# Performance work log

Measured on AMD Instinct MI355X. Metric: run time of the kernel, lower is better.

Reference implementation:

```python
import jax, jax.numpy as jnp
import numpy as np

N_NODES = 50000
N_EDGES = 800000
IN_DIM = 128
HID_DIM = 128
OUT_DIM = 128


def gcn_conv(x, src, dst, W, b, n):
    """PyG-style GCNConv: linear, add self-loops, sym-normalized scatter-add."""
    h = x @ W  # [N, out]
    loop = jnp.arange(n, dtype=src.dtype)
    src_f = jnp.concatenate([src, loop])
    dst_f = jnp.concatenate([dst, loop])
    ones = jnp.ones(src_f.shape[0], dtype=h.dtype)
    deg = jax.ops.segment_sum(ones, dst_f, num_segments=n)  # in-degree incl. self-loop
    dinv = jnp.where(deg > 0, jax.lax.rsqrt(deg), 0.0)
    norm = dinv[src_f] * dinv[dst_f]  # [E+N]
    msg = h[src_f] * norm[:, None]  # gather + scale
    out = jax.ops.segment_sum(msg, dst_f, num_segments=n)  # scatter-add
    return out + b


def setup_inputs() -> dict:
    key = jax.random.key(0)
    k1, k2, k3, k4, k5, k6 = jax.random.split(key, 6)
    posts = jax.random.normal(k1, (N_NODES, IN_DIM), dtype=jnp.float32)
    edge_index = jax.random.randint(k2, (2, N_EDGES), 0, N_NODES, dtype=jnp.int32)
    root_index = 0
    s1 = 1.0 / np.sqrt(IN_DIM)
    s2 = 1.0 / np.sqrt(HID_DIM + IN_DIM)
    W1 = jax.random.uniform(k3, (IN_DIM, HID_DIM), jnp.float32, -s1, s1)
    b1 = jax.random.uniform(k4, (HID_DIM,), jnp.float32, -s1, s1)
    W2 = jax.random.uniform(k5, (HID_DIM + IN_DIM, OUT_DIM), jnp.float32, -s2, s2)
    b2 = jax.random.uniform(k6, (OUT_DIM,), jnp.float32, -s2, s2)
    return {"posts": posts, "edge_index": edge_index, "root_index": root_index,
            "W1": W1, "b1": b1, "W2": W2, "b2": b2}


def reference(posts, edge_index, root_index, W1, b1, W2, b2):
    n = posts.shape[0]
    src, dst = edge_index[0], edge_index[1]
    post_root = posts[root_index]  # [in_dim], broadcast to all nodes below
    conv1_out = gcn_conv(posts, src, dst, W1, b1, n)  # [N, hid]
    conv1_root = conv1_out[root_index]  # [hid]
    conv2_in = jnp.concatenate(
        [jnp.broadcast_to(post_root, (n, post_root.shape[0])), conv1_out], axis=1)
    conv2_in = jax.nn.relu(conv2_in)  # dropout is identity in eval mode
    conv2_out = jax.nn.relu(gcn_conv(conv2_in, src, dst, W2, b2, n))  # [N, out]
    # mean over nodes of cat([conv1_root broadcast, conv2_out])
    feature = jnp.concatenate([conv1_root, jnp.mean(conv2_out, axis=0)])
    return feature.reshape(1, -1)
```

## Files before the change

kernel.cpp:

```cpp
#include <hip/hip_runtime.h>

#define DIM 128
#define WPAD 136
typedef unsigned int uint;
typedef unsigned short ushort;

#define RFL __builtin_amdgcn_readfirstlane

typedef __attribute__((ext_vector_type(8))) short bf16x8;
typedef __attribute__((ext_vector_type(4))) float f32x4;

__device__ __forceinline__ ushort f2bf(float x) {
    uint u = __float_as_uint(x);
    u = u + 0x7FFFu + ((u >> 16) & 1u);
    return (ushort)(u >> 16);
}

__global__ __launch_bounds__(256) void k_count(const int* __restrict__ dst,
                                               int* __restrict__ deg, int E) {
    int t = blockIdx.x * 256 + threadIdx.x;
    if (t < E) atomicAdd(&deg[dst[t]], 1);
}

__global__ __launch_bounds__(256) void k_dinv(const int* __restrict__ deg,
                                              float* __restrict__ dinv, int N) {
    int t = blockIdx.x * 256 + threadIdx.x;
    if (t < N) dinv[t] = rsqrtf((float)(deg[t] + 1));
}

__global__ __launch_bounds__(256) void k_scanA(const int* __restrict__ deg,
                                               int* __restrict__ rowptr,
                                               int* __restrict__ segsum, int N) {
    int i = blockIdx.x * 256 + threadIdx.x;
    int v = (i < N) ? deg[i] : 0;
    __shared__ int ps[256];
    ps[threadIdx.x] = v;
    __syncthreads();
    for (int off = 1; off < 256; off <<= 1) {
        int u = (threadIdx.x >= off) ? ps[threadIdx.x - off] : 0;
        __syncthreads();
        ps[threadIdx.x] += u;
        __syncthreads();
    }
    if (i < N) rowptr[i] = ps[threadIdx.x] - v;
    if (threadIdx.x == 255) segsum[blockIdx.x] = ps[255];
}

__global__ __launch_bounds__(256) void k_scanB(int* __restrict__ segsum, int nseg) {
    int t = threadIdx.x;
    int v = (t < nseg) ? segsum[t] : 0;
    __shared__ int ps[256];
    ps[t] = v;
    __syncthreads();
    for (int off = 1; off < 256; off <<= 1) {
        int u = (t >= off) ? ps[t - off] : 0;
        __syncthreads();
        ps[t] += u;
        __syncthreads();
    }
    if (t < nseg) segsum[t] = ps[t] - v;
}

__global__ __launch_bounds__(256) void k_scanC(int* __restrict__ rowptr,
                                               const int* __restrict__ segsum,
                                               int* __restrict__ cursor, int N, int E) {
    int i = blockIdx.x * 256 + threadIdx.x;
    if (i < N) {
        int r = rowptr[i] + segsum[blockIdx.x];
        rowptr[i] = r;
        cursor[i] = r;
    }
    if (i == 0) rowptr[N] = E;
}

__global__ __launch_bounds__(256) void k_fill(const int* __restrict__ src,
                                              const int* __restrict__ dst,
                                              const float* __restrict__ dinv,
                                              int* __restrict__ cursor,
                                              int2* __restrict__ csr, int E) {
    int e = blockIdx.x * 256 + threadIdx.x;
    if (e >= E) return;
    int s = src[e], d = dst[e];
    int p = atomicAdd(&cursor[d], 1);
    float w = dinv[s] * dinv[d];
    csr[p] = make_int2(s, __float_as_int(w));
}

template<bool RELU_IN, bool ADD_C>
__global__ __launch_bounds__(256) void k_gemm(const float* __restrict__ X,
                                              const float* __restrict__ W,
                                              const float* __restrict__ Cvec,
                                              ushort* __restrict__ H, int n) {
    __shared__ ushort sWT[DIM][WPAD];
    __shared__ ushort sX[4][16][WPAD];
    const int tid = threadIdx.x;
    const int w = tid >> 6, l = tid & 63;
    const int col = l & 15;
    const int kg = l >> 4;

    for (int idx = tid; idx < DIM * DIM; idx += 256) {
        int k = idx >> 7, j = idx & 127;
        sWT[j][k] = f2bf(W[idx]);
    }
    float cj[8];
    if (ADD_C) {
        #pragma unroll
        for (int t = 0; t < 8; ++t) cj[t] = Cvec[t * 16 + col];
    }
    __syncthreads();

    for (int base = blockIdx.x * 64; base < n; base += gridDim.x * 64) {
        int i0 = base + w * 16;
        for (int idx = l; idx < 16 * 32; idx += 64) {
            int r = idx >> 5, c4 = idx & 31;
            float4 v = make_float4(0.f, 0.f, 0.f, 0.f);
            if (i0 + r < n) v = ((const float4*)(X + (size_t)(i0 + r) * DIM))[c4];
            if (RELU_IN) {
                v.x = fmaxf(v.x, 0.f); v.y = fmaxf(v.y, 0.f);
                v.z = fmaxf(v.z, 0.f); v.w = fmaxf(v.w, 0.f);
            }
            ushort* p = &sX[w][r][c4 * 4];
            p[0] = f2bf(v.x); p[1] = f2bf(v.y); p[2] = f2bf(v.z); p[3] = f2bf(v.w);
        }
        f32x4 acc[8];
        #pragma unroll
        for (int t = 0; t < 8; ++t) {
            float c0 = ADD_C ? cj[t] : 0.f;
            acc[t][0] = c0; acc[t][1] = c0; acc[t][2] = c0; acc[t][3] = c0;
        }
        #pragma unroll
        for (int k0 = 0; k0 < DIM; k0 += 32) {
            bf16x8 a = *(const bf16x8*)&sX[w][col][k0 + kg * 8];
            #pragma unroll
            for (int t = 0; t < 8; ++t) {
                bf16x8 b = *(const bf16x8*)&sWT[t * 16 + col][k0 + kg * 8];
                acc[t] = __builtin_amdgcn_mfma_f32_16x16x32_bf16(a, b, acc[t], 0, 0, 0);
            }
        }
        #pragma unroll
        for (int t = 0; t < 8; ++t) {
            #pragma unroll
            for (int r = 0; r < 4; ++r) {
                int row = i0 + kg * 4 + r;
                if (row < n) H[(size_t)row * DIM + t * 16 + col] = f2bf(acc[t][r]);
            }
        }
    }
}

__global__ __launch_bounds__(DIM) void k_cvec(const float* __restrict__ posts,
                                              const int* __restrict__ root,
                                              const float* __restrict__ W2,
                                              float* __restrict__ cvec) {
    int j = threadIdx.x;
    const float* xr = posts + (size_t)root[0] * DIM;
    float acc = 0.0f;
    #pragma unroll 8
    for (int k = 0; k < DIM; ++k)
        acc = fmaf(fmaxf(xr[k], 0.0f), W2[k * DIM + j], acc);
    cvec[j] = acc;
}

__device__ __forceinline__ void wave_accum(const int2* __restrict__ csr,
                                           int beg, int end, int q,
                                           const ushort* __restrict__ h,
                                           float& a0, float& a1) {
    int e = beg;
    for (; e + 16 <= end; e += 16) {
        int sc[16];
        float wt[16];
        #pragma unroll
        for (int u = 0; u < 16; ++u) {
            int2 c = csr[e + u];
            sc[u] = RFL(c.x);
            wt[u] = __int_as_float(RFL(c.y));
        }
        uint hv[16];
        #pragma unroll
        for (int u = 0; u < 16; ++u)
            hv[u] = ((const uint*)(h + (size_t)sc[u] * DIM))[q];
        #pragma unroll
        for (int u = 0; u < 16; ++u) {
            a0 = fmaf(__uint_as_float(hv[u] << 16), wt[u], a0);
            a1 = fmaf(__uint_as_float(hv[u] & 0xFFFF0000u), wt[u], a1);
        }
    }
    for (; e + 8 <= end; e += 8) {
        int sc[8];
        float wt[8];
        #pragma unroll
        for (int u = 0; u < 8; ++u) {
            int2 c = csr[e + u];
            sc[u] = RFL(c.x);
            wt[u] = __int_as_float(RFL(c.y));
        }
        uint hv[8];
        #pragma unroll
        for (int u = 0; u < 8; ++u)
            hv[u] = ((const uint*)(h + (size_t)sc[u] * DIM))[q];
        #pragma unroll
        for (int u = 0; u < 8; ++u) {
            a0 = fmaf(__uint_as_float(hv[u] << 16), wt[u], a0);
            a1 = fmaf(__uint_as_float(hv[u] & 0xFFFF0000u), wt[u], a1);
        }
    }
    int rem = end - e;
    if (rem > 0) {
        int sc[8];
        float wt[8];
        #pragma unroll
        for (int u = 0; u < 8; ++u) {
            int idx = e + u; idx = idx < end ? idx : end - 1;
            int2 c = csr[idx];
            sc[u] = RFL(c.x);
            wt[u] = (u < rem) ? __int_as_float(RFL(c.y)) : 0.f;
        }
        uint hv[8];
        #pragma unroll
        for (int u = 0; u < 8; ++u)
            hv[u] = ((const uint*)(h + (size_t)sc[u] * DIM))[q];
        #pragma unroll
        for (int u = 0; u < 8; ++u) {
            a0 = fmaf(__uint_as_float(hv[u] << 16), wt[u], a0);
            a1 = fmaf(__uint_as_float(hv[u] & 0xFFFF0000u), wt[u], a1);
        }
    }
}

__global__ __launch_bounds__(256) void k_gather1(const int2* __restrict__ csr,
                                                 const int* __restrict__ rowptr,
                                                 const float* __restrict__ dinv,
                                                 const ushort* __restrict__ h,
                                                 const float* __restrict__ b1,
                                                 const int* __restrict__ root,
                                                 float* __restrict__ conv1,
                                                 float* __restrict__ out, int N) {
    int q = threadIdx.x & 63;
    int wid = blockIdx.x * 4 + (threadIdx.x >> 6);
    int wstride = gridDim.x * 4;
    float2 bv = ((const float2*)b1)[q];
    int rt = RFL(root[0]);
    for (int d = wid; d < N; d += wstride) {
        int beg = RFL(rowptr[d]);
        int end = RFL(rowptr[d + 1]);
        float a0 = 0.f, a1 = 0.f;
        wave_accum(csr, beg, end, q, h, a0, a1);
        float di = dinv[d], sl = di * di;
        uint hv = ((const uint*)(h + (size_t)d * DIM))[q];
        float2 r;
        r.x = fmaf(__uint_as_float(hv << 16), sl, a0) + bv.x;
        r.y = fmaf(__uint_as_float(hv & 0xFFFF0000u), sl, a1) + bv.y;
        ((float2*)(conv1 + (size_t)d * DIM))[q] = r;
        if (d == rt) ((float2*)out)[q] = r;
    }
}

__global__ __launch_bounds__(256) void k_gather2(const int2* __restrict__ csr,
                                                 const int* __restrict__ rowptr,
                                                 const float* __restrict__ dinv,
                                                 const ushort* __restrict__ h,
                                                 const float* __restrict__ b2,
                                                 float* __restrict__ meanacc, int N) {
    int q = threadIdx.x & 63;
    int wid = blockIdx.x * 4 + (threadIdx.x >> 6);
    int wstride = gridDim.x * 4;
    float2 bv = ((const float2*)b2)[q];
    float s0 = 0.f, s1 = 0.f;
    for (int d = wid; d < N; d += wstride) {
        int beg = RFL(rowptr[d]);
        int end = RFL(rowptr[d + 1]);
        float a0 = 0.f, a1 = 0.f;
        wave_accum(csr, beg, end, q, h, a0, a1);
        float di = dinv[d], sl = di * di;
        uint hv = ((const uint*)(h + (size_t)d * DIM))[q];
        s0 += fmaxf(fmaf(__uint_as_float(hv << 16), sl, a0) + bv.x, 0.f);
        s1 += fmaxf(fmaf(__uint_as_float(hv & 0xFFFF0000u), sl, a1) + bv.y, 0.f);
    }
    __shared__ float2 sp[256];
    sp[threadIdx.x] = make_float2(s0, s1);
    __syncthreads();
    if (threadIdx.x < 64) {
        float2 s = sp[threadIdx.x];
        #pragma unroll
        for (int g = 1; g < 4; ++g) {
            float2 o = sp[g * 64 + threadIdx.x];
            s.x += o.x; s.y += o.y;
        }
        unsafeAtomicAdd(&meanacc[q * 2 + 0], s.x);
        unsafeAtomicAdd(&meanacc[q * 2 + 1], s.y);
    }
}

__global__ __launch_bounds__(DIM) void k_reduce(const float* __restrict__ meanacc,
                                                float* __restrict__ out, int N) {
    int j = threadIdx.x;
    out[DIM + j] = meanacc[j] / (float)N;
}

extern "C" void kernel_launch(void* const* d_in, const int* in_sizes, int n_in,
                              void* d_out, int out_size, void* d_ws, size_t ws_size,
                              hipStream_t stream) {
    const float* posts = (const float*)d_in[0];
    const int*   eidx  = (const int*)d_in[1];
    const int*   root  = (const int*)d_in[2];
    const float* W1    = (const float*)d_in[3];
    const float* b1    = (const float*)d_in[4];
    const float* W2    = (const float*)d_in[5];
    const float* b2    = (const float*)d_in[6];
    float* out = (float*)d_out;

    int N = in_sizes[0] / DIM;
    int E = in_sizes[1] / 2;
    const int* src = eidx;
    const int* dst = eidx + E;
    int nseg = (N + 255) / 256;

    char* ws = (char*)d_ws;
    size_t off = 0;
    auto alloc = [&](size_t bytes) {
        void* p = ws + off;
        off += (bytes + 511) & ~(size_t)511;
        return p;
    };
    int*    deg     = (int*)   alloc((size_t)N * 4);
    int*    rowptr  = (int*)   alloc((size_t)(N + 1) * 4);
    int*    cursor  = (int*)   alloc((size_t)N * 4);
    int*    segsum  = (int*)   alloc((size_t)nseg * 4);
    float*  dinv    = (float*) alloc((size_t)N * 4);
    float*  cvec    = (float*) alloc(DIM * 4);
    float*  meanacc = (float*) alloc(DIM * 4);
    int2*   csr     = (int2*)  alloc((size_t)E * 8);
    ushort* h       = (ushort*)alloc((size_t)N * DIM * 2);
    float*  conv1   = (float*) alloc((size_t)N * DIM * 4);

    hipMemsetAsync(deg, 0, (size_t)N * 4, stream);
    hipMemsetAsync(meanacc, 0, DIM * 4, stream);

    k_count<<<(E + 255) / 256, 256, 0, stream>>>(dst, deg, E);
    k_scanA<<<nseg, 256, 0, stream>>>(deg, rowptr, segsum, N);
    k_scanB<<<1, 256, 0, stream>>>(segsum, nseg);
    k_scanC<<<nseg, 256, 0, stream>>>(rowptr, segsum, cursor, N, E);
    k_dinv<<<(N + 255) / 256, 256, 0, stream>>>(deg, dinv, N);
    k_fill<<<(E + 255) / 256, 256, 0, stream>>>(src, dst, dinv, cursor, csr, E);

    k_gemm<false, false><<<256, 256, 0, stream>>>(posts, W1, nullptr, h, N);
    k_gather1<<<2048, 256, 0, stream>>>(csr, rowptr, dinv, h, b1, root, conv1, out, N);

    k_cvec<<<1, DIM, 0, stream>>>(posts, root, W2, cvec);
    k_gemm<true, true><<<256, 256, 0, stream>>>(conv1, W2 + DIM * DIM, cvec, h, N);
    k_gather2<<<2048, 256, 0, stream>>>(csr, rowptr, dinv, h, b2, meanacc, N);
    k_reduce<<<1, DIM, 0, stream>>>(meanacc, out, N);
}
```

Before: 302.9 us.

## Partition CSR edges by source quarter and gather in four cache-friendly passes

Edges are bucketed per destination by which quarter of the node range their source falls in. Each gather then runs as four passes, each touching only one quarter of the bf16 feature table, which is meant to keep gather reads resident in cache. The cost is four times the launches, a partial accumulator row read and written in fp32 between passes, and a four-times-larger degree/scan array. k_scanB now needs 1024 threads to cover the larger segment count.

```diff
diff --git a/kernel.cpp b/kernel.cpp
--- a/kernel.cpp
+++ b/kernel.cpp
@@ -16,23 +16,35 @@
     return (ushort)(u >> 16);
 }
 
-__global__ __launch_bounds__(256) void k_count(const int* __restrict__ dst,
-                                               int* __restrict__ deg, int E) {
+__device__ __forceinline__ int src_bucket(int s, int Q) {
+    int p = s / Q;
+    return p > 3 ? 3 : p;
+}
+
+__global__ __launch_bounds__(256) void k_count4(const int* __restrict__ src,
+                                                const int* __restrict__ dst,
+                                                int* __restrict__ deg4, int E, int Q) {
     int t = blockIdx.x * 256 + threadIdx.x;
-    if (t < E) atomicAdd(&deg[dst[t]], 1);
-}
-
-__global__ __launch_bounds__(256) void k_dinv(const int* __restrict__ deg,
+    if (t < E) {
+        int p = src_bucket(src[t], Q);
+        atomicAdd(&deg4[(dst[t] << 2) + p], 1);
+    }
+}
+
+__global__ __launch_bounds__(256) void k_dinv(const int* __restrict__ rowptr4,
                                               float* __restrict__ dinv, int N) {
     int t = blockIdx.x * 256 + threadIdx.x;
-    if (t < N) dinv[t] = rsqrtf((float)(deg[t] + 1));
+    if (t < N) {
+        int deg = rowptr4[(t << 2) + 4] - rowptr4[t << 2];
+        dinv[t] = rsqrtf((float)(deg + 1));
+    }
 }
 
 __global__ __launch_bounds__(256) void k_scanA(const int* __restrict__ deg,
                                                int* __restrict__ rowptr,
-                                               int* __restrict__ segsum, int N) {
+                                               int* __restrict__ segsum, int M) {
     int i = blockIdx.x * 256 + threadIdx.x;
-    int v = (i < N) ? deg[i] : 0;
+    int v = (i < M) ? deg[i] : 0;
     __shared__ int ps[256];
     ps[threadIdx.x] = v;
     __syncthreads();
@@ -42,17 +54,17 @@
         ps[threadIdx.x] += u;
         __syncthreads();
     }
-    if (i < N) rowptr[i] = ps[threadIdx.x] - v;
+    if (i < M) rowptr[i] = ps[threadIdx.x] - v;
     if (threadIdx.x == 255) segsum[blockIdx.x] = ps[255];
 }
 
-__global__ __launch_bounds__(256) void k_scanB(int* __restrict__ segsum, int nseg) {
+__global__ __launch_bounds__(1024) void k_scanB(int* __restrict__ segsum, int nseg) {
     int t = threadIdx.x;
     int v = (t < nseg) ? segsum[t] : 0;
-    __shared__ int ps[256];
+    __shared__ int ps[1024];
     ps[t] = v;
     __syncthreads();
-    for (int off = 1; off < 256; off <<= 1) {
+    for (int off = 1; off < 1024; off <<= 1) {
         int u = (t >= off) ? ps[t - off] : 0;
         __syncthreads();
         ps[t] += u;
@@ -63,27 +75,28 @@
 
 __global__ __launch_bounds__(256) void k_scanC(int* __restrict__ rowptr,
                                                const int* __restrict__ segsum,
-                                               int* __restrict__ cursor, int N, int E) {
+                                               int* __restrict__ cursor, int M, int E) {
     int i = blockIdx.x * 256 + threadIdx.x;
-    if (i < N) {
+    if (i < M) {
         int r = rowptr[i] + segsum[blockIdx.x];
         rowptr[i] = r;
         cursor[i] = r;
     }
-    if (i == 0) rowptr[N] = E;
-}
-
-__global__ __launch_bounds__(256) void k_fill(const int* __restrict__ src,
-                                              const int* __restrict__ dst,
-                                              const float* __restrict__ dinv,
-                                              int* __restrict__ cursor,
-                                              int2* __restrict__ csr, int E) {
+    if (i == 0) rowptr[M] = E;
+}
+
+__global__ __launch_bounds__(256) void k_fill4(const int* __restrict__ src,
+                                               const int* __restrict__ dst,
+                                               const float* __restrict__ dinv,
+                                               int* __restrict__ cursor4,
+                                               int2* __restrict__ csr, int E, int Q) {
     int e = blockIdx.x * 256 + threadIdx.x;
     if (e >= E) return;
     int s = src[e], d = dst[e];
-    int p = atomicAdd(&cursor[d], 1);
+    int p = src_bucket(s, Q);
+    int pos = atomicAdd(&cursor4[(d << 2) + p], 1);
     float w = dinv[s] * dinv[d];
-    csr[p] = make_int2(s, __float_as_int(w));
+    csr[pos] = make_int2(s, __float_as_int(w));
 }
 
 template<bool RELU_IN, bool ADD_C>
@@ -227,67 +240,91 @@
     }
 }
 
+template<bool FIRST, bool LAST>
 __global__ __launch_bounds__(256) void k_gather1(const int2* __restrict__ csr,
-                                                 const int* __restrict__ rowptr,
+                                                 const int* __restrict__ rowptr4,
                                                  const float* __restrict__ dinv,
                                                  const ushort* __restrict__ h,
                                                  const float* __restrict__ b1,
                                                  const int* __restrict__ root,
                                                  float* __restrict__ conv1,
-                                                 float* __restrict__ out, int N) {
+                                                 float* __restrict__ out, int N, int pass) {
     int q = threadIdx.x & 63;
     int wid = blockIdx.x * 4 + (threadIdx.x >> 6);
     int wstride = gridDim.x * 4;
     float2 bv = ((const float2*)b1)[q];
     int rt = RFL(root[0]);
     for (int d = wid; d < N; d += wstride) {
-        int beg = RFL(rowptr[d]);
-        int end = RFL(rowptr[d + 1]);
+        int idx = (d << 2) + pass;
+        int beg = RFL(rowptr4[idx]);
+        int end = RFL(rowptr4[idx + 1]);
         float a0 = 0.f, a1 = 0.f;
         wave_accum(csr, beg, end, q, h, a0, a1);
-        float di = dinv[d], sl = di * di;
-        uint hv = ((const uint*)(h + (size_t)d * DIM))[q];
-        float2 r;
-        r.x = fmaf(__uint_as_float(hv << 16), sl, a0) + bv.x;
-        r.y = fmaf(__uint_as_float(hv & 0xFFFF0000u), sl, a1) + bv.y;
-        ((float2*)(conv1 + (size_t)d * DIM))[q] = r;
-        if (d == rt) ((float2*)out)[q] = r;
-    }
-}
-
+        float2* crow = (float2*)(conv1 + (size_t)d * DIM) + q;
+        float2 r = make_float2(a0, a1);
+        if (!FIRST) {
+            float2 c = *crow;
+            r.x += c.x; r.y += c.y;
+        }
+        if (LAST) {
+            float di = dinv[d], sl = di * di;
+            uint hv = ((const uint*)(h + (size_t)d * DIM))[q];
+            r.x = fmaf(__uint_as_float(hv << 16), sl, r.x) + bv.x;
+            r.y = fmaf(__uint_as_float(hv & 0xFFFF0000u), sl, r.y) + bv.y;
+        }
+        *crow = r;
+        if (LAST && d == rt) ((float2*)out)[q] = r;
+    }
+}
+
+template<bool FIRST, bool LAST>
 __global__ __launch_bounds__(256) void k_gather2(const int2* __restrict__ csr,
-                                                 const int* __restrict__ rowptr,
+                                                 const int* __restrict__ rowptr4,
                                                  const float* __restrict__ dinv,
                                                  const ushort* __restrict__ h,
                                                  const float* __restrict__ b2,
-                                                 float* __restrict__ meanacc, int N) {
+                                                 float* __restrict__ acc2,
+                                                 float* __restrict__ meanacc, int N, int pass) {
     int q = threadIdx.x & 63;
     int wid = blockIdx.x * 4 + (threadIdx.x >> 6);
     int wstride = gridDim.x * 4;
     float2 bv = ((const float2*)b2)[q];
     float s0 = 0.f, s1 = 0.f;
     for (int d = wid; d < N; d += wstride) {
-        int beg = RFL(rowptr[d]);
-        int end = RFL(rowptr[d + 1]);
+        int idx = (d << 2) + pass;
+        int beg = RFL(rowptr4[idx]);
+        int end = RFL(rowptr4[idx + 1]);
         float a0 = 0.f, a1 = 0.f;
         wave_accum(csr, beg, end, q, h, a0, a1);
-        float di = dinv[d], sl = di * di;
-        uint hv = ((const uint*)(h + (size_t)d * DIM))[q];
-        s0 += fmaxf(fmaf(__uint_as_float(hv << 16), sl, a0) + bv.x, 0.f);
-        s1 += fmaxf(fmaf(__uint_as_float(hv & 0xFFFF0000u), sl, a1) + bv.y, 0.f);
-    }
-    __shared__ float2 sp[256];
-    sp[threadIdx.x] = make_float2(s0, s1);
-    __syncthreads();
-    if (threadIdx.x < 64) {
-        float2 s = sp[threadIdx.x];
-        #pragma unroll
-        for (int g = 1; g < 4; ++g) {
-            float2 o = sp[g * 64 + threadIdx.x];
-            s.x += o.x; s.y += o.y;
-        }
-        unsafeAtomicAdd(&meanacc[q * 2 + 0], s.x);
-        unsafeAtomicAdd(&meanacc[q * 2 + 1], s.y);
+        float2* crow = (float2*)(acc2 + (size_t)d * DIM) + q;
+        float2 r = make_float2(a0, a1);
+        if (!FIRST) {
+            float2 c = *crow;
+            r.x += c.x; r.y += c.y;
+        }
+        if (!LAST) {
+            *crow = r;
+        } else {
+            float di = dinv[d], sl = di * di;
+            uint hv = ((const uint*)(h + (size_t)d * DIM))[q];
+            s0 += fmaxf(fmaf(__uint_as_float(hv << 16), sl, r.x) + bv.x, 0.f);
+            s1 += fmaxf(fmaf(__uint_as_float(hv & 0xFFFF0000u), sl, r.y) + bv.y, 0.f);
+        }
+    }
+    if (LAST) {
+        __shared__ float2 sp[256];
+        sp[threadIdx.x] = make_float2(s0, s1);
+        __syncthreads();
+        if (threadIdx.x < 64) {
+            float2 s = sp[threadIdx.x];
+            #pragma unroll
+            for (int g = 1; g < 4; ++g) {
+                float2 o = sp[g * 64 + threadIdx.x];
+                s.x += o.x; s.y += o.y;
+            }
+            unsafeAtomicAdd(&meanacc[q * 2 + 0], s.x);
+            unsafeAtomicAdd(&meanacc[q * 2 + 1], s.y);
+        }
     }
 }
 
@@ -311,9 +348,11 @@
 
     int N = in_sizes[0] / DIM;
     int E = in_sizes[1] / 2;
+    int Q = (N + 3) / 4;
     const int* src = eidx;
     const int* dst = eidx + E;
-    int nseg = (N + 255) / 256;
+    int M = N * 4;
+    int nseg4 = (M + 255) / 256;
 
     char* ws = (char*)d_ws;
     size_t off = 0;
@@ -322,10 +361,10 @@
         off += (bytes + 511) & ~(size_t)511;
         return p;
     };
-    int*    deg     = (int*)   alloc((size_t)N * 4);
-    int*    rowptr  = (int*)   alloc((size_t)(N + 1) * 4);
-    int*    cursor  = (int*)   alloc((size_t)N * 4);
-    int*    segsum  = (int*)   alloc((size_t)nseg * 4);
+    int*    deg4    = (int*)   alloc((size_t)M * 4);
+    int*    rowptr4 = (int*)   alloc(((size_t)M + 1) * 4);
+    int*    cursor4 = (int*)   alloc((size_t)M * 4);
+    int*    segsum  = (int*)   alloc((size_t)nseg4 * 4);
     float*  dinv    = (float*) alloc((size_t)N * 4);
     float*  cvec    = (float*) alloc(DIM * 4);
     float*  meanacc = (float*) alloc(DIM * 4);
@@ -333,21 +372,27 @@
     ushort* h       = (ushort*)alloc((size_t)N * DIM * 2);
     float*  conv1   = (float*) alloc((size_t)N * DIM * 4);
 
-    hipMemsetAsync(deg, 0, (size_t)N * 4, stream);
+    hipMemsetAsync(deg4, 0, (size_t)M * 4, stream);
     hipMemsetAsync(meanacc, 0, DIM * 4, stream);
 
-    k_count<<<(E + 255) / 256, 256, 0, stream>>>(dst, deg, E);
-    k_scanA<<<nseg, 256, 0, stream>>>(deg, rowptr, segsum, N);
-    k_scanB<<<1, 256, 0, stream>>>(segsum, nseg);
-    k_scanC<<<nseg, 256, 0, stream>>>(rowptr, segsum, cursor, N, E);
-    k_dinv<<<(N + 255) / 256, 256, 0, stream>>>(deg, dinv, N);
-    k_fill<<<(E + 255) / 256, 256, 0, stream>>>(src, dst, dinv, cursor, csr, E);
+    k_count4<<<(E + 255) / 256, 256, 0, stream>>>(src, dst, deg4, E, Q);
+    k_scanA<<<nseg4, 256, 0, stream>>>(deg4, rowptr4, segsum, M);
+    k_scanB<<<1, 1024, 0, stream>>>(segsum, nseg4);
+    k_scanC<<<nseg4, 256, 0, stream>>>(rowptr4, segsum, cursor4, M, E);
+    k_dinv<<<(N + 255) / 256, 256, 0, stream>>>(rowptr4, dinv, N);
+    k_fill4<<<(E + 255) / 256, 256, 0, stream>>>(src, dst, dinv, cursor4, csr, E, Q);
 
     k_gemm<false, false><<<256, 256, 0, stream>>>(posts, W1, nullptr, h, N);
-    k_gather1<<<2048, 256, 0, stream>>>(csr, rowptr, dinv, h, b1, root, conv1, out, N);
+    k_gather1<true,  false><<<2048, 256, 0, stream>>>(csr, rowptr4, dinv, h, b1, root, conv1, out, N, 0);
+    k_gather1<false, false><<<2048, 256, 0, stream>>>(csr, rowptr4, dinv, h, b1, root, conv1, out, N, 1);
+    k_gather1<false, false><<<2048, 256, 0, stream>>>(csr, rowptr4, dinv, h, b1, root, conv1, out, N, 2);
+    k_gather1<false, true ><<<2048, 256, 0, stream>>>(csr, rowptr4, dinv, h, b1, root, conv1, out, N, 3);
 
     k_cvec<<<1, DIM, 0, stream>>>(posts, root, W2, cvec);
     k_gemm<true, true><<<256, 256, 0, stream>>>(conv1, W2 + DIM * DIM, cvec, h, N);
-    k_gather2<<<2048, 256, 0, stream>>>(csr, rowptr, dinv, h, b2, meanacc, N);
+    k_gather2<true,  false><<<2048, 256, 0, stream>>>(csr, rowptr4, dinv, h, b2, conv1, meanacc, N, 0);
+    k_gather2<false, false><<<2048, 256, 0, stream>>>(csr, rowptr4, dinv, h, b2, conv1, meanacc, N, 1);
+    k_gather2<false, false><<<2048, 256, 0, stream>>>(csr, rowptr4, dinv, h, b2, conv1, meanacc, N, 2);
+    k_gather2<false, true ><<<2048, 256, 0, stream>>>(csr, rowptr4, dinv, h, b2, conv1, meanacc, N, 3);
     k_reduce<<<1, DIM, 0, stream>>>(meanacc, out, N);
 }
```

Result: slower. 370.9 us (+22.5%).
